# Kernel optimization log

Measured on AMD Instinct MI355X. Metric: run time of the kernel, lower is better.

The kernel has to match this reference:

```python
import jax, jax.numpy as jnp
import numpy as np


def setup_inputs() -> dict:
    key = jax.random.key(0)
    kq, kk, kv, km = jax.random.split(key, 4)
    B, H, S, D = 2, 16, 2048, 64
    Q = jax.random.normal(kq, (B, H, S, D), dtype=jnp.float32)
    K = jax.random.normal(kk, (B, H, S, D), dtype=jnp.float32)
    V = jax.random.normal(kv, (B, H, S, D), dtype=jnp.float32)
    mask = jax.random.randint(km, (B, 1, S, S), 0, 2).astype(jnp.bool_)
    return {"Q": Q, "K": K, "V": V, "mask": mask}


def reference(Q, K, V, mask):
    # scores: [B, H, Sq, Sk]
    scores = jnp.einsum("bhqd,bhkd->bhqk", Q, K)
    neg = jnp.finfo(scores.dtype).min
    # Faithful to original: mask fill happens BEFORE the sqrt(d) scaling.
    scores = jnp.where(mask, neg, scores)
    inv_sqrt_d = 1.0 / jnp.sqrt(jnp.asarray(Q.shape[-1], dtype=scores.dtype))
    attn = jax.nn.softmax(scores * inv_sqrt_d, axis=-1)
    return jnp.einsum("bhqk,bhkd->bhqd", attn, V)
```

## Files before the change

### kernel.cpp

```cpp
#include <hip/hip_runtime.h>
#include <stdint.h>


#define SQ 2048
#define DH 64

using bf16x8  = __attribute__((ext_vector_type(8)))  __bf16;
using f32x16  = __attribute__((ext_vector_type(16))) float;
using ushort8 = __attribute__((ext_vector_type(8)))  unsigned short;
using ushort4v= __attribute__((ext_vector_type(4)))  unsigned short;
using ushort2v= __attribute__((ext_vector_type(2)))  unsigned short;
using u32x4   = __attribute__((ext_vector_type(4)))  unsigned int;

static __device__ __forceinline__ unsigned short f2bf(float f) {
    union { float f; uint32_t u; } c; c.f = f;
    return (unsigned short)((c.u + 0x8000u) >> 16);
}

static __device__ __forceinline__ uint32_t pkbf(float a, float b) {
    union { __bf16 h[2]; uint32_t u; } t;
    t.h[0] = (__bf16)a; t.h[1] = (__bf16)b;
    return t.u;
}

static __device__ __forceinline__ f32x16 mfma32(bf16x8 a, bf16x8 b, f32x16 c) {
    return __builtin_amdgcn_mfma_f32_32x32x16_bf16(a, b, c, 0, 0, 0);
}

static __device__ __forceinline__ void gload16(const void* g, void* l) {
    __builtin_amdgcn_global_load_lds(
        (const __attribute__((address_space(1))) void*)g,
        (__attribute__((address_space(3))) void*)l, 16, 0, 0);
}

__global__ __launch_bounds__(256)
void prep_kernel(const int* __restrict__ mask, const float* __restrict__ K,
                 const float* __restrict__ V, unsigned long long* __restrict__ words,
                 unsigned short* __restrict__ Kb, unsigned short* __restrict__ Vt) {
    __shared__ unsigned short tl[64][66];
    const int bx  = blockIdx.x;
    const int tid = threadIdx.x;
    if (bx < 32768) {
        int gid = bx * 256 + tid;
        int mv = mask[gid];
        unsigned long long b = __ballot(mv != 0);
        if ((gid & 63) == 0) words[gid >> 6] = b;
    } else if (bx < 36864) {
        int gid = (bx - 32768) * 256 + tid;
        float4 v = ((const float4*)K)[gid];
        ushort4v t;
        t[0]=f2bf(v.x); t[1]=f2bf(v.y); t[2]=f2bf(v.z); t[3]=f2bf(v.w);
        ((ushort4v*)Kb)[gid] = t;
    } else {
        const int vbx = bx - 36864;
        const int kt  = vbx & 31;
        const size_t bh = vbx >> 5;
        const float* vp = V + (bh * SQ + (size_t)kt * 64) * DH;
        #pragma unroll
        for (int i = 0; i < 4; ++i) {
            int idx = tid + 256 * i;
            int key = idx >> 4;
            int dc  = (idx & 15) * 4;
            float4 v = *(const float4*)(vp + (size_t)key * DH + dc);
            tl[key][dc + 0] = f2bf(v.x);
            tl[key][dc + 1] = f2bf(v.y);
            tl[key][dc + 2] = f2bf(v.z);
            tl[key][dc + 3] = f2bf(v.w);
        }
        __syncthreads();
        unsigned short* op = Vt + bh * DH * SQ + (size_t)kt * 64;
        #pragma unroll
        for (int i = 0; i < 4; ++i) {
            int idx = tid + 256 * i;
            int d  = idx >> 4;
            int m  = idx & 15;
            int kc = m * 4;
            int base = 32 * ((m >> 3) & 1) + 8 * (m & 1) + 4 * ((m >> 2) & 1) + 2 * ((m >> 1) & 1);
            ushort2v w0, w1;
            w0[0] = tl[kc + 0][d]; w0[1] = tl[kc + 1][d];
            w1[0] = tl[kc + 2][d]; w1[1] = tl[kc + 3][d];
            *(ushort2v*)(op + (size_t)d * SQ + base)      = w0;
            *(ushort2v*)(op + (size_t)d * SQ + base + 16) = w1;
        }
    }
}

__global__ __launch_bounds__(256, 4)
void attn_kernel(const float* __restrict__ Q,
                 const unsigned short* __restrict__ Kb,
                 const unsigned short* __restrict__ Vtg,
                 const unsigned long long* __restrict__ Mw,
                 float* __restrict__ out) {
    __shared__ __align__(16) unsigned short Ks[2][64 * 64];
    __shared__ __align__(16) unsigned short Vs[2][64 * 64];

    const int tid  = threadIdx.x;
    const int w    = tid >> 6;
    const int l    = tid & 63;
    const int qh   = w >> 1;
    const int kh   = w & 1;
    const int q5   = l & 31;
    const int h    = l >> 5;
    const int bx = blockIdx.x;
    const int hh = bx & 15;
    const int b  = (bx >> 4) & 1;
    const int qt = bx >> 5;

    const size_t bh = (size_t)b * 16 + hh;
    const float* Qp = Q + bh * SQ * DH;
    const int qbase = qt * 64 + 32 * qh;

    const unsigned int* Mrow32 =
        (const unsigned int*)(Mw + ((size_t)b * SQ + qbase + q5) * (SQ / 64)) + kh;

    const int s0 = (2 * w) * 64 + l;
    const int s1 = (2 * w + 1) * 64 + l;
    const int r0 = s0 >> 3, g0s = s0 & 7;
    const int r1 = s1 >> 3, g1s = s1 & 7;
    const char* Kg = (const char*)(Kb  + bh * (size_t)SQ * DH);
    const char* Vg = (const char*)(Vtg + bh * (size_t)DH * SQ);
    const char* kSrc0 = Kg + r0 * 128  + ((g0s ^ (r0 & 7)) << 4);
    const char* kSrc1 = Kg + r1 * 128  + ((g1s ^ (r1 & 7)) << 4);
    const char* vSrc0 = Vg + r0 * 4096 + ((g0s ^ (r0 & 7)) << 4);
    const char* vSrc1 = Vg + r1 * 4096 + ((g1s ^ (r1 & 7)) << 4);

    bf16x8 qf[4];
    {
        const float* qr = Qp + (size_t)(qbase + q5) * DH;
        #pragma unroll
        for (int c = 0; c < 4; ++c) {
            int d0 = 16 * c + 8 * h;
            float4 a  = *(const float4*)(qr + d0);
            float4 b4 = *(const float4*)(qr + d0 + 4);
            ushort8 t;
            t[0]=f2bf(a.x);  t[1]=f2bf(a.y);  t[2]=f2bf(a.z);  t[3]=f2bf(a.w);
            t[4]=f2bf(b4.x); t[5]=f2bf(b4.y); t[6]=f2bf(b4.z); t[7]=f2bf(b4.w);
            qf[c] = __builtin_bit_cast(bf16x8, t);
        }
    }

    const int kr = 32 * kh + q5;
    int kOff[4];
    #pragma unroll
    for (int c = 0; c < 4; ++c)
        kOff[c] = kr * 128 + (((2 * c + h) ^ (kr & 7)) << 4);
    int vOff[2][2];
    #pragma unroll
    for (int db = 0; db < 2; ++db) {
        int d = 32 * db + q5;
        #pragma unroll
        for (int c = 0; c < 2; ++c)
            vOff[db][c] = d * 128 + (((4 * kh + 2 * c + h) ^ (d & 7)) << 4);
    }

    f32x16 o[2];
    float lsum = 0.f;
    o[0] = (f32x16)(0.f); o[1] = (f32x16)(0.f);

    unsigned int mwh = Mrow32[0];
    gload16(kSrc0, &Ks[0][(2 * w) * 512]);
    gload16(kSrc1, &Ks[0][(2 * w + 1) * 512]);
    gload16(vSrc0, &Vs[0][(2 * w) * 512]);
    gload16(vSrc1, &Vs[0][(2 * w + 1) * 512]);
    kSrc0 += 8192; kSrc1 += 8192; vSrc0 += 128; vSrc1 += 128;
    __syncthreads();

    for (int t = 0; t < 32; ++t) {
        const int cur = t & 1;

        unsigned int nmwh = 0;
        if (t < 31) {
            gload16(kSrc0, &Ks[cur ^ 1][(2 * w) * 512]);
            gload16(kSrc1, &Ks[cur ^ 1][(2 * w + 1) * 512]);
            gload16(vSrc0, &Vs[cur ^ 1][(2 * w) * 512]);
            gload16(vSrc1, &Vs[cur ^ 1][(2 * w + 1) * 512]);
            kSrc0 += 8192; kSrc1 += 8192; vSrc0 += 128; vSrc1 += 128;
            nmwh = Mrow32[2 * (t + 1)];
        }

        const char* Kc = (const char*)Ks + cur * 8192;
        const char* Vc = (const char*)Vs + cur * 8192;

        f32x16 s = (f32x16)(0.f);
        __builtin_amdgcn_s_setprio(1);
        #pragma unroll
        for (int c = 0; c < 4; ++c) {
            bf16x8 kb = __builtin_bit_cast(bf16x8, *(const ushort8*)(Kc + kOff[c]));
            s = mfma32(kb, qf[c], s);
        }
        __builtin_amdgcn_s_setprio(0);

        const unsigned int mh = mwh >> (4 * h);
        float pv[16];
        float ts = 0.f;
        #pragma unroll
        for (int r = 0; r < 16; ++r) {
            const int sh_amt = (r & 3) + 8 * (r >> 2);
            float e = __builtin_amdgcn_exp2f(fmaf(s[r], 0.18033688f, -5.7707802f));
            pv[r] = ((mh >> sh_amt) & 1u) ? 0.0f : e;
            ts += pv[r];
        }
        lsum += ts;

        unsigned int pk[4][2];
        #pragma unroll
        for (int g = 0; g < 4; ++g) {
            pk[g][0] = pkbf(pv[4 * g + 0], pv[4 * g + 1]);
            pk[g][1] = pkbf(pv[4 * g + 2], pv[4 * g + 3]);
        }
        bf16x8 pa[2];
        #pragma unroll
        for (int c = 0; c < 2; ++c) {
            u32x4 tv;
            tv[0] = pk[0][c]; tv[1] = pk[1][c]; tv[2] = pk[2][c]; tv[3] = pk[3][c];
            pa[c] = __builtin_bit_cast(bf16x8, tv);
        }

        __builtin_amdgcn_s_setprio(1);
        #pragma unroll
        for (int db = 0; db < 2; ++db) {
            #pragma unroll
            for (int c = 0; c < 2; ++c) {
                bf16x8 vb = __builtin_bit_cast(bf16x8,
                    *(const ushort8*)(Vc + vOff[db][c]));
                o[db] = mfma32(vb, pa[c], o[db]);
            }
        }
        __builtin_amdgcn_s_setprio(0);

        __syncthreads();
        mwh = nmwh;
    }

    float lhalf = lsum;
    lhalf += __shfl_xor(lhalf, 32, 64);
    float* Ored = (float*)Ks;
    float* Lred = (float*)Vs;
    if (kh) {
        #pragma unroll
        for (int db = 0; db < 2; ++db) {
            #pragma unroll
            for (int g = 0; g < 4; ++g) {
                int d0  = 32 * db + 8 * g + 4 * h;
                int g16 = (d0 >> 2) ^ ((q5 & 7) << 1);
                float4 st;
                st.x = o[db][4 * g + 0]; st.y = o[db][4 * g + 1];
                st.z = o[db][4 * g + 2]; st.w = o[db][4 * g + 3];
                *(float4*)(Ored + qh * 2048 + q5 * 64 + g16 * 4) = st;
            }
        }
        if (h == 0) Lred[qh * 32 + q5] = lhalf;
    }
    __syncthreads();
    if (!kh) {
        const float rinv = 1.0f / (lhalf + Lred[qh * 32 + q5]);
        float* op = out + (bh * SQ + (size_t)(qbase + q5)) * DH;
        #pragma unroll
        for (int db = 0; db < 2; ++db) {
            #pragma unroll
            for (int g = 0; g < 4; ++g) {
                int d0  = 32 * db + 8 * g + 4 * h;
                int g16 = (d0 >> 2) ^ ((q5 & 7) << 1);
                float4 pv4 = *(const float4*)(Ored + qh * 2048 + q5 * 64 + g16 * 4);
                float4 st;
                st.x = (o[db][4 * g + 0] + pv4.x) * rinv;
                st.y = (o[db][4 * g + 1] + pv4.y) * rinv;
                st.z = (o[db][4 * g + 2] + pv4.z) * rinv;
                st.w = (o[db][4 * g + 3] + pv4.w) * rinv;
                *(float4*)(op + d0) = st;
            }
        }
    }
}

extern "C" void kernel_launch(void* const* d_in, const int* in_sizes, int n_in,
                              void* d_out, int out_size, void* d_ws, size_t ws_size,
                              hipStream_t stream) {
    const float* Q    = (const float*)d_in[0];
    const float* K    = (const float*)d_in[1];
    const float* V    = (const float*)d_in[2];
    const int*   mask = (const int*)d_in[3];
    float* out = (float*)d_out;

    char* ws = (char*)d_ws;
    unsigned long long* mwords = (unsigned long long*)ws;
    unsigned short* Kb = (unsigned short*)(ws + (1 << 20));
    unsigned short* Vt = (unsigned short*)(ws + (1 << 20) + (8 << 20));

    prep_kernel<<<dim3(37888), dim3(256), 0, stream>>>(mask, K, V, mwords, Kb, Vt);
    attn_kernel<<<dim3(1024), dim3(256), 0, stream>>>(Q, Kb, Vt, mwords, out);
}
```

Baseline: 183.3 us.

## Software-pipeline QK and PV across tiles with triple-buffered V

Restructures the main loop so the QK^T MFMAs for tile t are issued alongside the PV MFMAs for tile t-1, using a two-stage register handoff of packed probabilities and a rotating triple buffer for V in shared memory. The softmax scale is folded into Q when it is converted to bf16, so the per-element FMA before exp2 goes away and the constant offset is dropped. The cross-wave output reduction now uses a padded row layout instead of an XOR swizzle. LDS use grows to 40 KB per block, which may affect occupancy, and without the offset exp2 is more exposed to overflow on large scores.

```diff
diff --git a/kernel.cpp b/kernel.cpp
--- a/kernel.cpp
+++ b/kernel.cpp
@@ -91,8 +91,9 @@
                  const unsigned short* __restrict__ Vtg,
                  const unsigned long long* __restrict__ Mw,
                  float* __restrict__ out) {
-    __shared__ __align__(16) unsigned short Ks[2][64 * 64];
-    __shared__ __align__(16) unsigned short Vs[2][64 * 64];
+    __shared__ __align__(16) char smem[40960];
+    char* KsBase = smem;
+    char* VsBase = smem + 16384;
 
     const int tid  = threadIdx.x;
     const int w    = tid >> 6;
@@ -124,6 +125,7 @@
     const char* vSrc0 = Vg + r0 * 4096 + ((g0s ^ (r0 & 7)) << 4);
     const char* vSrc1 = Vg + r1 * 4096 + ((g1s ^ (r1 & 7)) << 4);
 
+    const float SC = 0.18033688f;
     bf16x8 qf[4];
     {
         const float* qr = Qp + (size_t)(qbase + q5) * DH;
@@ -133,8 +135,8 @@
             float4 a  = *(const float4*)(qr + d0);
             float4 b4 = *(const float4*)(qr + d0 + 4);
             ushort8 t;
-            t[0]=f2bf(a.x);  t[1]=f2bf(a.y);  t[2]=f2bf(a.z);  t[3]=f2bf(a.w);
-            t[4]=f2bf(b4.x); t[5]=f2bf(b4.y); t[6]=f2bf(b4.z); t[7]=f2bf(b4.w);
+            t[0]=f2bf(a.x*SC);  t[1]=f2bf(a.y*SC);  t[2]=f2bf(a.z*SC);  t[3]=f2bf(a.w*SC);
+            t[4]=f2bf(b4.x*SC); t[5]=f2bf(b4.y*SC); t[6]=f2bf(b4.z*SC); t[7]=f2bf(b4.w*SC);
             qf[c] = __builtin_bit_cast(bf16x8, t);
         }
     }
@@ -157,96 +159,130 @@
     float lsum = 0.f;
     o[0] = (f32x16)(0.f); o[1] = (f32x16)(0.f);
 
-    unsigned int mwh = Mrow32[0];
-    gload16(kSrc0, &Ks[0][(2 * w) * 512]);
-    gload16(kSrc1, &Ks[0][(2 * w + 1) * 512]);
-    gload16(vSrc0, &Vs[0][(2 * w) * 512]);
-    gload16(vSrc1, &Vs[0][(2 * w + 1) * 512]);
-    kSrc0 += 8192; kSrc1 += 8192; vSrc0 += 128; vSrc1 += 128;
-    __syncthreads();
-
-    for (int t = 0; t < 32; ++t) {
-        const int cur = t & 1;
-
-        unsigned int nmwh = 0;
-        if (t < 31) {
-            gload16(kSrc0, &Ks[cur ^ 1][(2 * w) * 512]);
-            gload16(kSrc1, &Ks[cur ^ 1][(2 * w + 1) * 512]);
-            gload16(vSrc0, &Vs[cur ^ 1][(2 * w) * 512]);
-            gload16(vSrc1, &Vs[cur ^ 1][(2 * w + 1) * 512]);
-            kSrc0 += 8192; kSrc1 += 8192; vSrc0 += 128; vSrc1 += 128;
-            nmwh = Mrow32[2 * (t + 1)];
-        }
-
-        const char* Kc = (const char*)Ks + cur * 8192;
-        const char* Vc = (const char*)Vs + cur * 8192;
-
+    auto stageTo = [&](int kbuf, int voff) {
+        gload16(kSrc0, KsBase + kbuf * 8192 + (2 * w) * 1024);
+        gload16(kSrc1, KsBase + kbuf * 8192 + (2 * w + 1) * 1024);
+        gload16(vSrc0, VsBase + voff + (2 * w) * 1024);
+        gload16(vSrc1, VsBase + voff + (2 * w + 1) * 1024);
+        kSrc0 += 8192; kSrc1 += 8192; vSrc0 += 128; vSrc1 += 128;
+    };
+    auto qk = [&](int kbuf) -> f32x16 {
         f32x16 s = (f32x16)(0.f);
         __builtin_amdgcn_s_setprio(1);
         #pragma unroll
         for (int c = 0; c < 4; ++c) {
-            bf16x8 kb = __builtin_bit_cast(bf16x8, *(const ushort8*)(Kc + kOff[c]));
+            bf16x8 kb = __builtin_bit_cast(bf16x8,
+                *(const ushort8*)(KsBase + kbuf * 8192 + kOff[c]));
             s = mfma32(kb, qf[c], s);
         }
         __builtin_amdgcn_s_setprio(0);
-
+        return s;
+    };
+    auto softmax_pack = [&](const f32x16& s, unsigned int mwh, bf16x8 (&pa)[2]) {
         const unsigned int mh = mwh >> (4 * h);
         float pv[16];
         float ts = 0.f;
         #pragma unroll
         for (int r = 0; r < 16; ++r) {
             const int sh_amt = (r & 3) + 8 * (r >> 2);
-            float e = __builtin_amdgcn_exp2f(fmaf(s[r], 0.18033688f, -5.7707802f));
+            float e = __builtin_amdgcn_exp2f(s[r]);
             pv[r] = ((mh >> sh_amt) & 1u) ? 0.0f : e;
             ts += pv[r];
         }
         lsum += ts;
-
         unsigned int pk[4][2];
         #pragma unroll
         for (int g = 0; g < 4; ++g) {
             pk[g][0] = pkbf(pv[4 * g + 0], pv[4 * g + 1]);
             pk[g][1] = pkbf(pv[4 * g + 2], pv[4 * g + 3]);
         }
-        bf16x8 pa[2];
         #pragma unroll
         for (int c = 0; c < 2; ++c) {
             u32x4 tv;
             tv[0] = pk[0][c]; tv[1] = pk[1][c]; tv[2] = pk[2][c]; tv[3] = pk[3][c];
             pa[c] = __builtin_bit_cast(bf16x8, tv);
         }
-
+    };
+    auto pvstep = [&](int voff, const bf16x8 (&pa)[2]) {
         __builtin_amdgcn_s_setprio(1);
         #pragma unroll
         for (int db = 0; db < 2; ++db) {
             #pragma unroll
             for (int c = 0; c < 2; ++c) {
                 bf16x8 vb = __builtin_bit_cast(bf16x8,
-                    *(const ushort8*)(Vc + vOff[db][c]));
+                    *(const ushort8*)(VsBase + voff + vOff[db][c]));
                 o[db] = mfma32(vb, pa[c], o[db]);
             }
         }
         __builtin_amdgcn_s_setprio(0);
-
-        __syncthreads();
-        mwh = nmwh;
-    }
+    };
+
+    int voff_prev = 16384, voff_cur = 0, voff_next = 8192;
+    auto rot = [&]() {
+        int tmp = voff_prev; voff_prev = voff_cur; voff_cur = voff_next; voff_next = tmp;
+    };
+
+    bf16x8 paA[2], paB[2];
+    unsigned int mwA = Mrow32[0], mwB;
+
+    stageTo(0, voff_cur);
+    __syncthreads();
+
+    stageTo(1, voff_next);
+    mwB = Mrow32[2];
+    {
+        f32x16 s = qk(0);
+        softmax_pack(s, mwA, paA);
+    }
+    __syncthreads();
+    rot();
+
+    #pragma unroll 1
+    for (int tp = 0; tp < 15; ++tp) {
+        {
+            const int t = 2 * tp + 1;
+            stageTo(0, voff_next);
+            mwA = Mrow32[2 * (t + 1)];
+            f32x16 s = qk(1);
+            pvstep(voff_prev, paA);
+            softmax_pack(s, mwB, paB);
+            __syncthreads();
+            rot();
+        }
+        {
+            const int t = 2 * tp + 2;
+            stageTo(1, voff_next);
+            mwB = Mrow32[2 * (t + 1)];
+            f32x16 s = qk(0);
+            pvstep(voff_prev, paB);
+            softmax_pack(s, mwA, paA);
+            __syncthreads();
+            rot();
+        }
+    }
+    {
+        f32x16 s = qk(1);
+        pvstep(voff_prev, paA);
+        softmax_pack(s, mwB, paB);
+    }
+    pvstep(voff_cur, paB);
+    __syncthreads();
 
     float lhalf = lsum;
     lhalf += __shfl_xor(lhalf, 32, 64);
-    float* Ored = (float*)Ks;
-    float* Lred = (float*)Vs;
+    float* Ored = (float*)smem;
+    float* Lred = (float*)(smem + 2 * 32 * 68 * 4);
     if (kh) {
+        float* row = Ored + (qh * 32 + q5) * 68;
         #pragma unroll
         for (int db = 0; db < 2; ++db) {
             #pragma unroll
             for (int g = 0; g < 4; ++g) {
-                int d0  = 32 * db + 8 * g + 4 * h;
-                int g16 = (d0 >> 2) ^ ((q5 & 7) << 1);
+                int d0 = 32 * db + 8 * g + 4 * h;
                 float4 st;
                 st.x = o[db][4 * g + 0]; st.y = o[db][4 * g + 1];
                 st.z = o[db][4 * g + 2]; st.w = o[db][4 * g + 3];
-                *(float4*)(Ored + qh * 2048 + q5 * 64 + g16 * 4) = st;
+                *(float4*)(row + d0) = st;
             }
         }
         if (h == 0) Lred[qh * 32 + q5] = lhalf;
@@ -254,14 +290,14 @@
     __syncthreads();
     if (!kh) {
         const float rinv = 1.0f / (lhalf + Lred[qh * 32 + q5]);
+        const float* row = Ored + (qh * 32 + q5) * 68;
         float* op = out + (bh * SQ + (size_t)(qbase + q5)) * DH;
         #pragma unroll
         for (int db = 0; db < 2; ++db) {
             #pragma unroll
             for (int g = 0; g < 4; ++g) {
-                int d0  = 32 * db + 8 * g + 4 * h;
-                int g16 = (d0 >> 2) ^ ((q5 & 7) << 1);
-                float4 pv4 = *(const float4*)(Ored + qh * 2048 + q5 * 64 + g16 * 4);
+                int d0 = 32 * db + 8 * g + 4 * h;
+                float4 pv4 = *(const float4*)(row + d0);
                 float4 st;
                 st.x = (o[db][4 * g + 0] + pv4.x) * rinv;
                 st.y = (o[db][4 * g + 1] + pv4.y) * rinv;
```

Result: faster. 176.3 us (-3.8%).
